# Optimization experiments

Measured on AMD Instinct MI355X. Metric: run time of the kernel, lower is better.

The kernel has to match this reference:

```python
import jax, jax.numpy as jnp
import numpy as np

VOCAB, EMB_DIM, HIDDEN, NUM_CLASSES = 50000, 300, 1000, 5
B, MAX_LEN = 4096, 128


def setup_inputs() -> dict:
    key = jax.random.key(0)
    k1, k2, k3, k4, k5, k6, k7 = jax.random.split(key, 7)
    x = jax.random.randint(k1, (B, MAX_LEN), 0, VOCAB, dtype=jnp.int64)
    lengths = jnp.maximum(jax.random.randint(k2, (B,), 0, MAX_LEN, dtype=jnp.int64), 1)
    emb_table = jax.random.normal(k3, (VOCAB, EMB_DIM), dtype=jnp.float32) * 0.1
    W1 = jax.random.normal(k4, (2 * EMB_DIM, HIDDEN), dtype=jnp.float32) * (1.0 / np.sqrt(2 * EMB_DIM))
    b1 = jax.random.normal(k5, (HIDDEN,), dtype=jnp.float32) * 0.01
    W2 = jax.random.normal(k6, (HIDDEN, NUM_CLASSES), dtype=jnp.float32) * (1.0 / np.sqrt(HIDDEN))
    b2 = jax.random.normal(k7, (NUM_CLASSES,), dtype=jnp.float32) * 0.01
    return {"x": x, "lengths": lengths, "emb_table": emb_table,
            "W1": W1, "b1": b1, "W2": W2, "b2": b2}


def reference(x, lengths, emb_table, W1, b1, W2, b2):
    emb = emb_table[x]                                  # [B, L, D] gather
    mask = (jnp.arange(emb.shape[1])[None, :] < lengths[:, None])  # [B, L]
    m = mask[:, :, None].astype(emb.dtype)
    avg_pool = jnp.sum(emb * m, axis=1) / lengths[:, None].astype(emb.dtype)  # [B, D]
    neg_inf = jnp.finfo(emb.dtype).min
    max_pool = jnp.max(jnp.where(mask[:, :, None], emb, neg_inf), axis=1)     # [B, D]
    rep = jnp.concatenate([avg_pool, max_pool], axis=1)  # [B, 2D]
    hidden = jax.nn.relu(rep @ W1 + b1)                  # [B, 1000]
    logits = hidden @ W2 + b2                            # [B, C]
    return logits
```

## Files before the change

kernel.cpp:

```cpp
#include <hip/hip_runtime.h>
#include <float.h>
#include <stdint.h>

#define EMB_DIM  300
#define MAX_LEN  128
#define HIDDEN   1000
#define NCLS     5
#define VOCAB_SZ 50000
#define KPAD     640
#define NPAD     1024
#define EMBPAD   320

typedef float    f32x4  __attribute__((ext_vector_type(4)));
typedef __bf16   bf16x8 __attribute__((ext_vector_type(8)));
typedef unsigned short ushort8v __attribute__((ext_vector_type(8)));

#define CONV_BLOCKS ((VOCAB_SZ * (EMBPAD / 4) + 255) / 256)

__device__ __forceinline__ unsigned short f2bf(float f) {
    union { float f; uint32_t u; } v; v.f = f;
    uint32_t u = v.u;
    return (unsigned short)((u + 0x7FFFu + ((u >> 16) & 1u)) >> 16);
}
__device__ __forceinline__ float bf2f(unsigned short h) {
    union { uint32_t u; float f; } v; v.u = ((uint32_t)h) << 16;
    return v.f;
}

__global__ __launch_bounds__(256) void prep_all(
    const float* __restrict__ emb, unsigned short* __restrict__ embb,
    const float* __restrict__ W1, unsigned short* __restrict__ Bt,
    const float* __restrict__ W2, unsigned short* __restrict__ W2t)
{
    __shared__ float t[32][33];
    const int blk = blockIdx.x;

    if (blk < CONV_BLOCKS) {
        const int i = blk * 256 + threadIdx.x;
        if (i >= VOCAB_SZ * (EMBPAD / 4)) return;
        const int v  = i / (EMBPAD / 4);
        const int ch = i - v * (EMBPAD / 4);
        ushort4 o = {0, 0, 0, 0};
        if (ch < 75) {
            const float4 f = *(const float4*)(emb + (size_t)v * EMB_DIM + ch * 4);
            o.x = f2bf(f.x); o.y = f2bf(f.y); o.z = f2bf(f.z); o.w = f2bf(f.w);
        }
        *(ushort4*)(embb + (size_t)v * EMBPAD + ch * 4) = o;
        return;
    }
    const int pb = blk - CONV_BLOCKS;
    if (pb >= 640) {
        const int i = (pb - 640) * 256 + threadIdx.x;
        const int c = i >> 10, k = i & 1023;
        const float v = (k < HIDDEN) ? W2[(size_t)k * NCLS + c] : 0.f;
        W2t[(size_t)c * 1024 + k] = f2bf(v);
        return;
    }
    const int px = pb & 31, py = pb >> 5;
    const int tx = threadIdx.x & 31, ty = threadIdx.x >> 5;
    const int n0 = px * 32, k0 = py * 32;
    #pragma unroll
    for (int i = 0; i < 4; ++i) {
        int k = k0 + ty + i * 8, n = n0 + tx;
        t[ty + i * 8][tx] = (k < 600 && n < HIDDEN) ? W1[(size_t)k * HIDDEN + n] : 0.f;
    }
    __syncthreads();
    #pragma unroll
    for (int i = 0; i < 4; ++i) {
        int n = n0 + ty + i * 8, k = k0 + tx;
        Bt[(size_t)n * KPAD + k] = f2bf(t[tx][ty + i * 8]);
    }
}

__global__ __launch_bounds__(128) void pool_bf16(
    const int* __restrict__ x, const int* __restrict__ lengths,
    const unsigned short* __restrict__ embb, unsigned short* __restrict__ rep)
{
    const int b = blockIdx.x;
    const int t = threadIdx.x;

    __shared__ int sidx[MAX_LEN];
    sidx[t] = x[b * MAX_LEN + t];
    __syncthreads();

    unsigned short* rb = rep + (size_t)b * KPAD;

    if (t >= 75) {
        if (t < 85) {
            ushort4 z = {0, 0, 0, 0};
            *(ushort4*)(rb + 600 + (t - 75) * 4) = z;
        }
        return;
    }

    int L = lengths[b];
    L = max(1, min(L, MAX_LEN));

    const int d = t * 4;
    float4 s  = {0.f, 0.f, 0.f, 0.f};
    float4 mx = {-FLT_MAX, -FLT_MAX, -FLT_MAX, -FLT_MAX};

    int i = 0;
    for (; i + 2 <= L; i += 2) {
        int i0 = max(0, min(sidx[i],     VOCAB_SZ - 1));
        int i1 = max(0, min(sidx[i + 1], VOCAB_SZ - 1));
        const ushort4 a = *(const ushort4*)(embb + (size_t)i0 * EMBPAD + d);
        const ushort4 c = *(const ushort4*)(embb + (size_t)i1 * EMBPAD + d);
        float a0 = bf2f(a.x), a1 = bf2f(a.y), a2 = bf2f(a.z), a3 = bf2f(a.w);
        float c0 = bf2f(c.x), c1 = bf2f(c.y), c2 = bf2f(c.z), c3 = bf2f(c.w);
        s.x += a0 + c0; s.y += a1 + c1; s.z += a2 + c2; s.w += a3 + c3;
        mx.x = fmaxf(mx.x, fmaxf(a0, c0)); mx.y = fmaxf(mx.y, fmaxf(a1, c1));
        mx.z = fmaxf(mx.z, fmaxf(a2, c2)); mx.w = fmaxf(mx.w, fmaxf(a3, c3));
    }
    if (i < L) {
        int i0 = max(0, min(sidx[i], VOCAB_SZ - 1));
        const ushort4 a = *(const ushort4*)(embb + (size_t)i0 * EMBPAD + d);
        float a0 = bf2f(a.x), a1 = bf2f(a.y), a2 = bf2f(a.z), a3 = bf2f(a.w);
        s.x += a0; s.y += a1; s.z += a2; s.w += a3;
        mx.x = fmaxf(mx.x, a0); mx.y = fmaxf(mx.y, a1);
        mx.z = fmaxf(mx.z, a2); mx.w = fmaxf(mx.w, a3);
    }

    const float inv = 1.0f / (float)L;
    ushort4 av, mv;
    av.x = f2bf(s.x * inv); av.y = f2bf(s.y * inv);
    av.z = f2bf(s.z * inv); av.w = f2bf(s.w * inv);
    mv.x = f2bf(mx.x); mv.y = f2bf(mx.y); mv.z = f2bf(mx.z); mv.w = f2bf(mx.w);
    *(ushort4*)(rb + d)       = av;
    *(ushort4*)(rb + 300 + d) = mv;
}

__global__ __launch_bounds__(128) void pool_f32(
    const int* __restrict__ x, const int* __restrict__ lengths,
    const float* __restrict__ emb, unsigned short* __restrict__ rep)
{
    const int b = blockIdx.x;
    const int t = threadIdx.x;

    __shared__ int sidx[MAX_LEN];
    sidx[t] = x[b * MAX_LEN + t];
    __syncthreads();

    unsigned short* rb = rep + (size_t)b * KPAD;

    if (t >= 75) {
        if (t < 85) {
            ushort4 z = {0, 0, 0, 0};
            *(ushort4*)(rb + 600 + (t - 75) * 4) = z;
        }
        return;
    }

    int L = lengths[b];
    L = max(1, min(L, MAX_LEN));

    const int d = t * 4;
    float4 s  = {0.f, 0.f, 0.f, 0.f};
    float4 mx = {-FLT_MAX, -FLT_MAX, -FLT_MAX, -FLT_MAX};

    for (int i = 0; i < L; ++i) {
        int idx = max(0, min(sidx[i], VOCAB_SZ - 1));
        const float4 v = *(const float4*)(emb + (size_t)idx * EMB_DIM + d);
        s.x += v.x; s.y += v.y; s.z += v.z; s.w += v.w;
        mx.x = fmaxf(mx.x, v.x); mx.y = fmaxf(mx.y, v.y);
        mx.z = fmaxf(mx.z, v.z); mx.w = fmaxf(mx.w, v.w);
    }

    const float inv = 1.0f / (float)L;
    ushort4 av, mv;
    av.x = f2bf(s.x * inv); av.y = f2bf(s.y * inv);
    av.z = f2bf(s.z * inv); av.w = f2bf(s.w * inv);
    mv.x = f2bf(mx.x); mv.y = f2bf(mx.y); mv.z = f2bf(mx.z); mv.w = f2bf(mx.w);
    *(ushort4*)(rb + d)       = av;
    *(ushort4*)(rb + 300 + d) = mv;
}

#define BM 64
#define BN 64
#define BK 64

__global__ __launch_bounds__(256, 4) void gemm1p(
    const unsigned short* __restrict__ A,
    const unsigned short* __restrict__ Bt,
    const float* __restrict__ bias,
    const unsigned short* __restrict__ W2t,
    float* __restrict__ partials,
    int M)
{
    __shared__ unsigned short As[2][BM * BK];
    __shared__ unsigned short Bs[2][BN * BK];

    const int tid  = threadIdx.x;
    const int wv   = tid >> 6;
    const int lane = tid & 63;
    const int bm   = blockIdx.y * BM;
    const int bn   = blockIdx.x * BN;
    const int wr   = (wv & 1) * 32;
    const int wc   = (wv >> 1) * 32;

    f32x4 acc[2][2] = {};

    auto stage = [&](int buf, int k0) {
        #pragma unroll
        for (int j = 0; j < 2; ++j) {
            int ci  = (wv * 2 + j) * 64 + lane;
            int row = ci >> 3, c = ci & 7;
            const unsigned short* g = A + (size_t)(bm + row) * KPAD + k0 + c * 8;
            unsigned short* l = &As[buf][(wv * 2 + j) * 512];
            __builtin_amdgcn_global_load_lds(g, l, 16, 0, 0);
        }
        #pragma unroll
        for (int j = 0; j < 2; ++j) {
            int ci  = (wv * 2 + j) * 64 + lane;
            int row = ci >> 3, c = ci & 7;
            const unsigned short* g = Bt + (size_t)(bn + row) * KPAD + k0 + c * 8;
            unsigned short* l = &Bs[buf][(wv * 2 + j) * 512];
            __builtin_amdgcn_global_load_lds(g, l, 16, 0, 0);
        }
    };

    stage(0, 0);
    int cur = 0;
    const int q = lane >> 4, r16 = lane & 15;

    #pragma unroll 1
    for (int it = 0; it < KPAD / BK; ++it) {
        __syncthreads();
        if (it + 1 < KPAD / BK) stage(cur ^ 1, (it + 1) * BK);

        #pragma unroll
        for (int ks = 0; ks < BK; ks += 32) {
            bf16x8 af[2], bfr[2];
            #pragma unroll
            for (int mi = 0; mi < 2; ++mi)
                af[mi] = *(const bf16x8*)&As[cur][(wr + mi * 16 + r16) * BK + ks + q * 8];
            #pragma unroll
            for (int nj = 0; nj < 2; ++nj)
                bfr[nj] = *(const bf16x8*)&Bs[cur][(wc + nj * 16 + r16) * BK + ks + q * 8];
            #pragma unroll
            for (int mi = 0; mi < 2; ++mi)
                #pragma unroll
                for (int nj = 0; nj < 2; ++nj)
                    acc[mi][nj] = __builtin_amdgcn_mfma_f32_16x16x32_bf16(
                        af[mi], bfr[nj], acc[mi][nj], 0, 0, 0);
        }
        cur ^= 1;
    }

    float bv[2], w2v[2][NCLS];
    #pragma unroll
    for (int nj = 0; nj < 2; ++nj) {
        int n = bn + wc + nj * 16 + r16;
        if (n < HIDDEN) {
            bv[nj] = bias[n];
            #pragma unroll
            for (int c = 0; c < NCLS; ++c) w2v[nj][c] = bf2f(W2t[c * 1024 + n]);
        } else {
            bv[nj] = 0.f;
            #pragma unroll
            for (int c = 0; c < NCLS; ++c) w2v[nj][c] = 0.f;
        }
    }

    __syncthreads();
    float* pl = (float*)As;

    #pragma unroll
    for (int mi = 0; mi < 2; ++mi) {
        #pragma unroll
        for (int r = 0; r < 4; ++r) {
            float p[NCLS] = {0.f, 0.f, 0.f, 0.f, 0.f};
            #pragma unroll
            for (int nj = 0; nj < 2; ++nj) {
                float h = fmaxf(acc[mi][nj][r] + bv[nj], 0.f);
                #pragma unroll
                for (int c = 0; c < NCLS; ++c) p[c] += h * w2v[nj][c];
            }
            #pragma unroll
            for (int off = 1; off < 16; off <<= 1)
                #pragma unroll
                for (int c = 0; c < NCLS; ++c)
                    p[c] += __shfl_xor(p[c], off, 64);
            if (r16 == 0) {
                int lr = mi * 16 + q * 4 + r;
                #pragma unroll
                for (int c = 0; c < NCLS; ++c)
                    pl[(wv * 32 + lr) * NCLS + c] = p[c];
            }
        }
    }
    __syncthreads();

    for (int e = tid; e < BM * NCLS; e += 256) {
        int lr = e / NCLS, c = e - lr * NCLS;
        float v;
        if (lr < 32) v = pl[(0 * 32 + lr) * NCLS + c] + pl[(2 * 32 + lr) * NCLS + c];
        else         v = pl[(1 * 32 + lr - 32) * NCLS + c] + pl[(3 * 32 + lr - 32) * NCLS + c];
        partials[(size_t)blockIdx.x * M * NCLS + (size_t)(bm + lr) * NCLS + c] = v;
    }
}

__global__ __launch_bounds__(256) void reduce_out(
    const float* __restrict__ partials, const float* __restrict__ b2,
    float* __restrict__ out, int M)
{
    const int i = blockIdx.x * 256 + threadIdx.x;
    if (i >= M * NCLS) return;
    const int c = i % NCLS;
    float s = b2[c];
    #pragma unroll
    for (int nb = 0; nb < NPAD / BN; ++nb)
        s += partials[(size_t)nb * M * NCLS + i];
    out[i] = s;
}

extern "C" void kernel_launch(void* const* d_in, const int* in_sizes, int n_in,
                              void* d_out, int out_size, void* d_ws, size_t ws_size,
                              hipStream_t stream)
{
    const int*   x       = (const int*)d_in[0];
    const int*   lengths = (const int*)d_in[1];
    const float* emb     = (const float*)d_in[2];
    const float* W1      = (const float*)d_in[3];
    const float* b1      = (const float*)d_in[4];
    const float* W2      = (const float*)d_in[5];
    const float* b2      = (const float*)d_in[6];
    float*       out     = (float*)d_out;

    const int B = in_sizes[1];

    unsigned short* rep      = (unsigned short*)d_ws;
    unsigned short* w1t      = rep + (size_t)B * KPAD;
    unsigned short* w2t      = w1t + (size_t)NPAD * KPAD;
    unsigned short* embb     = w2t + (size_t)NCLS * 1024;
    float*          partials = (float*)(embb + (size_t)VOCAB_SZ * EMBPAD);

    const size_t need = ((size_t)B * KPAD + (size_t)NPAD * KPAD + NCLS * 1024
                         + (size_t)VOCAB_SZ * EMBPAD) * 2
                        + (size_t)(NPAD / BN) * B * NCLS * 4;

    prep_all<<<CONV_BLOCKS + 660, 256, 0, stream>>>(emb, embb, W1, w1t, W2, w2t);

    if (ws_size >= need) {
        pool_bf16<<<B, 128, 0, stream>>>(x, lengths, embb, rep);
    } else {
        pool_f32<<<B, 128, 0, stream>>>(x, lengths, emb, rep);
    }

    dim3 g1(NPAD / BN, B / BM);
    gemm1p<<<g1, 256, 0, stream>>>(rep, w1t, b1, w2t, partials, B);

    reduce_out<<<(B * NCLS + 255) / 256, 256, 0, stream>>>(partials, b2, out, B);
}
```

Baseline: 161.8 us.

## Enlarge GEMM tiles, replace partial reduce with atomics, widen conversion and pooling unroll

The GEMM tile grows from 64x64 to 128x128 with a 4x4 MFMA accumulator per wave and two blocks per CU. It writes the fused second-layer results straight to the output with atomicAdd, and prep_all now initializes the output with b2. This removes the partials buffer and the separate reduce kernel launch, at the cost of fewer GEMM blocks (256) and atomic contention on each output element. The embedding bf16 conversion moves to 8-wide chunks, and pooling clamps indices once when loading them into shared memory and unrolls the gather loop by four for more loads in flight. Atomic accumulation makes the floating-point summation order nondeterministic.

After: 161.0 us. No clear change (-0.5%).

```diff
diff --git a/kernel.cpp b/kernel.cpp
--- a/kernel.cpp
+++ b/kernel.cpp
@@ -11,11 +11,12 @@
 #define NPAD     1024
 #define EMBPAD   320
 
-typedef float    f32x4  __attribute__((ext_vector_type(4)));
-typedef __bf16   bf16x8 __attribute__((ext_vector_type(8)));
+typedef float    f32x4   __attribute__((ext_vector_type(4)));
+typedef __bf16   bf16x8  __attribute__((ext_vector_type(8)));
 typedef unsigned short ushort8v __attribute__((ext_vector_type(8)));
 
-#define CONV_BLOCKS ((VOCAB_SZ * (EMBPAD / 4) + 255) / 256)
+#define EMB_CHUNKS (VOCAB_SZ * (EMBPAD / 8))
+#define EMB_BLOCKS ((EMB_CHUNKS + 255) / 256)
 
 __device__ __forceinline__ unsigned short f2bf(float f) {
     union { float f; uint32_t u; } v; v.f = f;
@@ -30,46 +31,60 @@
 __global__ __launch_bounds__(256) void prep_all(
     const float* __restrict__ emb, unsigned short* __restrict__ embb,
     const float* __restrict__ W1, unsigned short* __restrict__ Bt,
-    const float* __restrict__ W2, unsigned short* __restrict__ W2t)
+    const float* __restrict__ W2, unsigned short* __restrict__ W2t,
+    const float* __restrict__ b2, float* __restrict__ out,
+    int M, int embBlocks)
 {
     __shared__ float t[32][33];
     const int blk = blockIdx.x;
 
-    if (blk < CONV_BLOCKS) {
+    if (blk < embBlocks) {
         const int i = blk * 256 + threadIdx.x;
-        if (i >= VOCAB_SZ * (EMBPAD / 4)) return;
-        const int v  = i / (EMBPAD / 4);
-        const int ch = i - v * (EMBPAD / 4);
-        ushort4 o = {0, 0, 0, 0};
-        if (ch < 75) {
-            const float4 f = *(const float4*)(emb + (size_t)v * EMB_DIM + ch * 4);
-            o.x = f2bf(f.x); o.y = f2bf(f.y); o.z = f2bf(f.z); o.w = f2bf(f.w);
-        }
-        *(ushort4*)(embb + (size_t)v * EMBPAD + ch * 4) = o;
-        return;
-    }
-    const int pb = blk - CONV_BLOCKS;
-    if (pb >= 640) {
-        const int i = (pb - 640) * 256 + threadIdx.x;
+        if (i >= EMB_CHUNKS) return;
+        const int v  = i / 40;
+        const int ch = i - v * 40;
+        ushort8v o = {0, 0, 0, 0, 0, 0, 0, 0};
+        if (ch < 38) {
+            const float* src = emb + (size_t)v * EMB_DIM + ch * 8;
+            const float4 f0 = *(const float4*)src;
+            o[0] = f2bf(f0.x); o[1] = f2bf(f0.y); o[2] = f2bf(f0.z); o[3] = f2bf(f0.w);
+            if (ch < 37) {
+                const float4 f1 = *(const float4*)(src + 4);
+                o[4] = f2bf(f1.x); o[5] = f2bf(f1.y); o[6] = f2bf(f1.z); o[7] = f2bf(f1.w);
+            }
+        }
+        *(ushort8v*)(embb + (size_t)v * EMBPAD + ch * 8) = o;
+        return;
+    }
+    const int pb = blk - embBlocks;
+    if (pb < 640) {
+        const int px = pb & 31, py = pb >> 5;
+        const int tx = threadIdx.x & 31, ty = threadIdx.x >> 5;
+        const int n0 = px * 32, k0 = py * 32;
+        #pragma unroll
+        for (int i = 0; i < 4; ++i) {
+            int k = k0 + ty + i * 8, n = n0 + tx;
+            t[ty + i * 8][tx] = (k < 600 && n < HIDDEN) ? W1[(size_t)k * HIDDEN + n] : 0.f;
+        }
+        __syncthreads();
+        #pragma unroll
+        for (int i = 0; i < 4; ++i) {
+            int n = n0 + ty + i * 8, k = k0 + tx;
+            Bt[(size_t)n * KPAD + k] = f2bf(t[tx][ty + i * 8]);
+        }
+        return;
+    }
+    const int pc = pb - 640;
+    if (pc < 20) {
+        const int i = pc * 256 + threadIdx.x;
         const int c = i >> 10, k = i & 1023;
         const float v = (k < HIDDEN) ? W2[(size_t)k * NCLS + c] : 0.f;
         W2t[(size_t)c * 1024 + k] = f2bf(v);
         return;
     }
-    const int px = pb & 31, py = pb >> 5;
-    const int tx = threadIdx.x & 31, ty = threadIdx.x >> 5;
-    const int n0 = px * 32, k0 = py * 32;
-    #pragma unroll
-    for (int i = 0; i < 4; ++i) {
-        int k = k0 + ty + i * 8, n = n0 + tx;
-        t[ty + i * 8][tx] = (k < 600 && n < HIDDEN) ? W1[(size_t)k * HIDDEN + n] : 0.f;
-    }
-    __syncthreads();
-    #pragma unroll
-    for (int i = 0; i < 4; ++i) {
-        int n = n0 + ty + i * 8, k = k0 + tx;
-        Bt[(size_t)n * KPAD + k] = f2bf(t[tx][ty + i * 8]);
-    }
+    const int po = pc - 20;
+    const int oi = po * 256 + threadIdx.x;
+    if (oi < M * NCLS) out[oi] = b2[oi % NCLS];
 }
 
 __global__ __launch_bounds__(128) void pool_bf16(
@@ -80,7 +95,10 @@
     const int t = threadIdx.x;
 
     __shared__ int sidx[MAX_LEN];
-    sidx[t] = x[b * MAX_LEN + t];
+    {
+        int v = x[b * MAX_LEN + t];
+        sidx[t] = max(0, min(v, VOCAB_SZ - 1));
+    }
     __syncthreads();
 
     unsigned short* rb = rep + (size_t)b * KPAD;
@@ -97,25 +115,32 @@
     L = max(1, min(L, MAX_LEN));
 
     const int d = t * 4;
+    const unsigned short* base = embb + d;
     float4 s  = {0.f, 0.f, 0.f, 0.f};
     float4 mx = {-FLT_MAX, -FLT_MAX, -FLT_MAX, -FLT_MAX};
 
     int i = 0;
-    for (; i + 2 <= L; i += 2) {
-        int i0 = max(0, min(sidx[i],     VOCAB_SZ - 1));
-        int i1 = max(0, min(sidx[i + 1], VOCAB_SZ - 1));
-        const ushort4 a = *(const ushort4*)(embb + (size_t)i0 * EMBPAD + d);
-        const ushort4 c = *(const ushort4*)(embb + (size_t)i1 * EMBPAD + d);
-        float a0 = bf2f(a.x), a1 = bf2f(a.y), a2 = bf2f(a.z), a3 = bf2f(a.w);
-        float c0 = bf2f(c.x), c1 = bf2f(c.y), c2 = bf2f(c.z), c3 = bf2f(c.w);
-        s.x += a0 + c0; s.y += a1 + c1; s.z += a2 + c2; s.w += a3 + c3;
-        mx.x = fmaxf(mx.x, fmaxf(a0, c0)); mx.y = fmaxf(mx.y, fmaxf(a1, c1));
-        mx.z = fmaxf(mx.z, fmaxf(a2, c2)); mx.w = fmaxf(mx.w, fmaxf(a3, c3));
-    }
-    if (i < L) {
-        int i0 = max(0, min(sidx[i], VOCAB_SZ - 1));
-        const ushort4 a = *(const ushort4*)(embb + (size_t)i0 * EMBPAD + d);
-        float a0 = bf2f(a.x), a1 = bf2f(a.y), a2 = bf2f(a.z), a3 = bf2f(a.w);
+    for (; i + 4 <= L; i += 4) {
+        const ushort4 u0 = *(const ushort4*)(base + (size_t)sidx[i]     * EMBPAD);
+        const ushort4 u1 = *(const ushort4*)(base + (size_t)sidx[i + 1] * EMBPAD);
+        const ushort4 u2 = *(const ushort4*)(base + (size_t)sidx[i + 2] * EMBPAD);
+        const ushort4 u3 = *(const ushort4*)(base + (size_t)sidx[i + 3] * EMBPAD);
+        float a0 = bf2f(u0.x), a1 = bf2f(u0.y), a2 = bf2f(u0.z), a3 = bf2f(u0.w);
+        float b0 = bf2f(u1.x), b1v = bf2f(u1.y), b2v = bf2f(u1.z), b3 = bf2f(u1.w);
+        float c0 = bf2f(u2.x), c1 = bf2f(u2.y), c2 = bf2f(u2.z), c3 = bf2f(u2.w);
+        float e0 = bf2f(u3.x), e1 = bf2f(u3.y), e2 = bf2f(u3.z), e3 = bf2f(u3.w);
+        s.x += (a0 + b0) + (c0 + e0);
+        s.y += (a1 + b1v) + (c1 + e1);
+        s.z += (a2 + b2v) + (c2 + e2);
+        s.w += (a3 + b3) + (c3 + e3);
+        mx.x = fmaxf(mx.x, fmaxf(fmaxf(a0, b0), fmaxf(c0, e0)));
+        mx.y = fmaxf(mx.y, fmaxf(fmaxf(a1, b1v), fmaxf(c1, e1)));
+        mx.z = fmaxf(mx.z, fmaxf(fmaxf(a2, b2v), fmaxf(c2, e2)));
+        mx.w = fmaxf(mx.w, fmaxf(fmaxf(a3, b3), fmaxf(c3, e3)));
+    }
+    for (; i < L; ++i) {
+        const ushort4 u = *(const ushort4*)(base + (size_t)sidx[i] * EMBPAD);
+        float a0 = bf2f(u.x), a1 = bf2f(u.y), a2 = bf2f(u.z), a3 = bf2f(u.w);
         s.x += a0; s.y += a1; s.z += a2; s.w += a3;
         mx.x = fmaxf(mx.x, a0); mx.y = fmaxf(mx.y, a1);
         mx.z = fmaxf(mx.z, a2); mx.w = fmaxf(mx.w, a3);
@@ -175,16 +200,16 @@
     *(ushort4*)(rb + 300 + d) = mv;
 }
 
-#define BM 64
-#define BN 64
+#define BM 128
+#define BN 128
 #define BK 64
 
-__global__ __launch_bounds__(256, 4) void gemm1p(
+__global__ __launch_bounds__(256, 2) void gemm1p(
     const unsigned short* __restrict__ A,
     const unsigned short* __restrict__ Bt,
     const float* __restrict__ bias,
     const unsigned short* __restrict__ W2t,
-    float* __restrict__ partials,
+    float* __restrict__ out,
     int M)
 {
     __shared__ unsigned short As[2][BM * BK];
@@ -195,27 +220,27 @@
     const int lane = tid & 63;
     const int bm   = blockIdx.y * BM;
     const int bn   = blockIdx.x * BN;
-    const int wr   = (wv & 1) * 32;
-    const int wc   = (wv >> 1) * 32;
-
-    f32x4 acc[2][2] = {};
+    const int wr   = (wv & 1) * 64;
+    const int wc   = (wv >> 1) * 64;
+
+    f32x4 acc[4][4] = {};
 
     auto stage = [&](int buf, int k0) {
         #pragma unroll
-        for (int j = 0; j < 2; ++j) {
-            int ci  = (wv * 2 + j) * 64 + lane;
-            int row = ci >> 3, c = ci & 7;
-            const unsigned short* g = A + (size_t)(bm + row) * KPAD + k0 + c * 8;
-            unsigned short* l = &As[buf][(wv * 2 + j) * 512];
-            __builtin_amdgcn_global_load_lds(g, l, 16, 0, 0);
-        }
-        #pragma unroll
-        for (int j = 0; j < 2; ++j) {
-            int ci  = (wv * 2 + j) * 64 + lane;
-            int row = ci >> 3, c = ci & 7;
-            const unsigned short* g = Bt + (size_t)(bn + row) * KPAD + k0 + c * 8;
-            unsigned short* l = &Bs[buf][(wv * 2 + j) * 512];
-            __builtin_amdgcn_global_load_lds(g, l, 16, 0, 0);
+        for (int j = 0; j < 4; ++j) {
+            const int ci  = (wv * 4 + j) * 64 + lane;
+            const int row = ci >> 3, c = ci & 7;
+            __builtin_amdgcn_global_load_lds(
+                A + (size_t)(bm + row) * KPAD + k0 + c * 8,
+                &As[buf][(wv * 4 + j) * 512], 16, 0, 0);
+        }
+        #pragma unroll
+        for (int j = 0; j < 4; ++j) {
+            const int ci  = (wv * 4 + j) * 64 + lane;
+            const int row = ci >> 3, c = ci & 7;
+            __builtin_amdgcn_global_load_lds(
+                Bt + (size_t)(bn + row) * KPAD + k0 + c * 8,
+                &Bs[buf][(wv * 4 + j) * 512], 16, 0, 0);
         }
     };
 
@@ -230,27 +255,27 @@
 
         #pragma unroll
         for (int ks = 0; ks < BK; ks += 32) {
-            bf16x8 af[2], bfr[2];
-            #pragma unroll
-            for (int mi = 0; mi < 2; ++mi)
+            bf16x8 af[4], bfr[4];
+            #pragma unroll
+            for (int mi = 0; mi < 4; ++mi)
                 af[mi] = *(const bf16x8*)&As[cur][(wr + mi * 16 + r16) * BK + ks + q * 8];
             #pragma unroll
-            for (int nj = 0; nj < 2; ++nj)
+            for (int nj = 0; nj < 4; ++nj)
                 bfr[nj] = *(const bf16x8*)&Bs[cur][(wc + nj * 16 + r16) * BK + ks + q * 8];
             #pragma unroll
-            for (int mi = 0; mi < 2; ++mi)
+            for (int mi = 0; mi < 4; ++mi)
                 #pragma unroll
-                for (int nj = 0; nj < 2; ++nj)
+                for (int nj = 0; nj < 4; ++nj)
                     acc[mi][nj] = __builtin_amdgcn_mfma_f32_16x16x32_bf16(
                         af[mi], bfr[nj], acc[mi][nj], 0, 0, 0);
         }
         cur ^= 1;
     }
 
-    float bv[2], w2v[2][NCLS];
+    float bv[4], w2v[4][NCLS];
     #pragma unroll
-    for (int nj = 0; nj < 2; ++nj) {
-        int n = bn + wc + nj * 16 + r16;
+    for (int nj = 0; nj < 4; ++nj) {
+        const int n = bn + wc + nj * 16 + r16;
         if (n < HIDDEN) {
             bv[nj] = bias[n];
             #pragma unroll
@@ -266,12 +291,12 @@
     float* pl = (float*)As;
 
     #pragma unroll
-    for (int mi = 0; mi < 2; ++mi) {
+    for (int mi = 0; mi < 4; ++mi) {
         #pragma unroll
         for (int r = 0; r < 4; ++r) {
             float p[NCLS] = {0.f, 0.f, 0.f, 0.f, 0.f};
             #pragma unroll
-            for (int nj = 0; nj < 2; ++nj) {
+            for (int nj = 0; nj < 4; ++nj) {
                 float h = fmaxf(acc[mi][nj][r] + bv[nj], 0.f);
                 #pragma unroll
                 for (int c = 0; c < NCLS; ++c) p[c] += h * w2v[nj][c];
@@ -282,36 +307,22 @@
                 for (int c = 0; c < NCLS; ++c)
                     p[c] += __shfl_xor(p[c], off, 64);
             if (r16 == 0) {
-                int lr = mi * 16 + q * 4 + r;
+                const int lr = mi * 16 + q * 4 + r;
                 #pragma unroll
                 for (int c = 0; c < NCLS; ++c)
-                    pl[(wv * 32 + lr) * NCLS + c] = p[c];
+                    pl[(wv * 64 + lr) * NCLS + c] = p[c];
             }
         }
     }
     __syncthreads();
 
     for (int e = tid; e < BM * NCLS; e += 256) {
-        int lr = e / NCLS, c = e - lr * NCLS;
+        const int lr = e / NCLS, c = e - lr * NCLS;
         float v;
-        if (lr < 32) v = pl[(0 * 32 + lr) * NCLS + c] + pl[(2 * 32 + lr) * NCLS + c];
-        else         v = pl[(1 * 32 + lr - 32) * NCLS + c] + pl[(3 * 32 + lr - 32) * NCLS + c];
-        partials[(size_t)blockIdx.x * M * NCLS + (size_t)(bm + lr) * NCLS + c] = v;
-    }
-}
-
-__global__ __launch_bounds__(256) void reduce_out(
-    const float* __restrict__ partials, const float* __restrict__ b2,
-    float* __restrict__ out, int M)
-{
-    const int i = blockIdx.x * 256 + threadIdx.x;
-    if (i >= M * NCLS) return;
-    const int c = i % NCLS;
-    float s = b2[c];
-    #pragma unroll
-    for (int nb = 0; nb < NPAD / BN; ++nb)
-        s += partials[(size_t)nb * M * NCLS + i];
-    out[i] = s;
+        if (lr < 64) v = pl[(0 * 64 + lr)      * NCLS + c] + pl[(2 * 64 + lr)      * NCLS + c];
+        else         v = pl[(1 * 64 + lr - 64) * NCLS + c] + pl[(3 * 64 + lr - 64) * NCLS + c];
+        atomicAdd(out + (size_t)(bm + lr) * NCLS + c, v);
+    }
 }
 
 extern "C" void kernel_launch(void* const* d_in, const int* in_sizes, int n_in,
@@ -329,26 +340,27 @@
 
     const int B = in_sizes[1];
 
-    unsigned short* rep      = (unsigned short*)d_ws;
-    unsigned short* w1t      = rep + (size_t)B * KPAD;
-    unsigned short* w2t      = w1t + (size_t)NPAD * KPAD;
-    unsigned short* embb     = w2t + (size_t)NCLS * 1024;
-    float*          partials = (float*)(embb + (size_t)VOCAB_SZ * EMBPAD);
+    unsigned short* rep  = (unsigned short*)d_ws;
+    unsigned short* w1t  = rep + (size_t)B * KPAD;
+    unsigned short* w2t  = w1t + (size_t)NPAD * KPAD;
+    unsigned short* embb = w2t + (size_t)NCLS * 1024;
 
     const size_t need = ((size_t)B * KPAD + (size_t)NPAD * KPAD + NCLS * 1024
-                         + (size_t)VOCAB_SZ * EMBPAD) * 2
-                        + (size_t)(NPAD / BN) * B * NCLS * 4;
-
-    prep_all<<<CONV_BLOCKS + 660, 256, 0, stream>>>(emb, embb, W1, w1t, W2, w2t);
-
-    if (ws_size >= need) {
+                         + (size_t)VOCAB_SZ * EMBPAD) * 2;
+
+    const bool useBf16  = (ws_size >= need);
+    const int  embBlks  = useBf16 ? EMB_BLOCKS : 0;
+    const int  outBlks  = (B * NCLS + 255) / 256;
+
+    prep_all<<<embBlks + 660 + outBlks, 256, 0, stream>>>(
+        emb, embb, W1, w1t, W2, w2t, b2, out, B, embBlks);
+
+    if (useBf16) {
         pool_bf16<<<B, 128, 0, stream>>>(x, lengths, embb, rep);
     } else {
         pool_f32<<<B, 128, 0, stream>>>(x, lengths, emb, rep);
     }
 
     dim3 g1(NPAD / BN, B / BM);
-    gemm1p<<<g1, 256, 0, stream>>>(rep, w1t, b1, w2t, partials, B);
-
-    reduce_out<<<(B * NCLS + 255) / 256, 256, 0, stream>>>(partials, b2, out, B);
-}
+    gemm1p<<<g1, 256, 0, stream>>>(rep, w1t, b1, w2t, out, B);
+}
```
